# Performance work log

Measured on AMD Instinct MI355X. Metric: run time of the kernel, lower is better.

The kernel has to match this reference:

```python
import jax, jax.numpy as jnp
from jax import lax
import numpy as np

VOCAB, L, D, K = 50000, 8921, 300, 10
B, T = 8, 2048


def setup_inputs() -> dict:
    key = jax.random.key(0)
    k_ids, k_e, k_cw, k_cb, k_u = jax.random.split(key, 5)
    ids = jax.random.randint(k_ids, (B, T), 0, VOCAB, dtype=jnp.int32)
    embed_w = jax.random.normal(k_e, (VOCAB, D), dtype=jnp.float32) * 0.02
    embed_w = embed_w.at[0].set(0.0)  # padding_idx=0
    conv_w = jax.random.normal(k_cw, (D, D, K), dtype=jnp.float32) * 0.02  # (out, in, k) == torch OIH
    conv_b = jax.random.normal(k_cb, (D,), dtype=jnp.float32) * 0.02
    U = jax.random.normal(k_u, (L, D), dtype=jnp.float32)
    fc_bias = jnp.zeros((L,), dtype=jnp.float32)
    return {"ids": ids, "embed_w": embed_w, "conv_w": conv_w, "conv_b": conv_b, "U": U, "fc_bias": fc_bias}


def reference(ids, embed_w, conv_w, conv_b, U, fc_bias):
    # Embedding lookup (padding_idx row already zeroed in table)
    e = embed_w[ids]                       # (B, T, D)
    x = jnp.transpose(e, (0, 2, 1))        # (B, D, T)
    pad = conv_w.shape[-1] - 1             # torch padding=filter_size-1 (both sides)
    h = lax.conv_general_dilated(
        x, conv_w, window_strides=(1,), padding=[(pad, pad)],
        dimension_numbers=("NCH", "OIH", "NCH"))
    h = jax.nn.relu(h + conv_b[None, :, None])   # (B, D, T') where T' = T + K - 1
    attn = jax.nn.softmax(jnp.einsum("ld,bdt->blt", U, h), axis=-1)  # (B, L, T')
    z = jnp.einsum("blt,bdt->bld", attn, h)                          # (B, L, D)
    logits = jnp.einsum("bld,ld->bl", z, U) + fc_bias                # (B, L)
    return logits
```

## Files before the change

kernel.cpp:

```cpp
#include <hip/hip_runtime.h>

#define VOCAB   50000
#define LDIM    8921
#define DDIM    300
#define DPAD    320
#define KSZ     10
#define BATCH   8
#define TSEQ    2048
#define PADL    9
#define TPRIME  2057
#define TPADDED 2066
#define LPAD    8928

#define TSTG    32
#define NTT     65
#define TALLOC  (NTT * TSTG)
#define LBLK    70

typedef short s8v __attribute__((ext_vector_type(8)));
typedef float f4v __attribute__((ext_vector_type(4)));

typedef const __attribute__((address_space(1))) unsigned int* gas_ptr;
typedef __attribute__((address_space(3))) unsigned int* las_ptr;

__device__ inline unsigned short f2bf(float f) {
  union { float f; unsigned u; } v; v.f = f;
  unsigned r = v.u + 0x7FFF + ((v.u >> 16) & 1);
  return (unsigned short)(r >> 16);
}

__global__ __launch_bounds__(256) void gather_kernel(
    const int* __restrict__ ids, const float* __restrict__ embed_w,
    unsigned short* __restrict__ xp) {
  int wid = blockIdx.x * 4 + (threadIdx.x >> 6);
  int lane = threadIdx.x & 63;
  int b = wid / TPADDED, tau = wid % TPADDED;
  bool inr = (tau >= PADL) && (tau < PADL + TSEQ);
  int row = inr ? ids[b * TSEQ + (tau - PADL)] : 0;
  const float* src = embed_w + (size_t)row * DDIM;
  unsigned short* dst = xp + ((size_t)b * TPADDED + tau) * DPAD;
#pragma unroll
  for (int j = 0; j < 3; ++j) {
    int c2 = (j * 64 + lane) * 2;
    if (c2 < DPAD) {
      float v0 = (inr && c2 < DDIM) ? src[c2] : 0.0f;
      float v1 = (inr && c2 + 1 < DDIM) ? src[c2 + 1] : 0.0f;
      unsigned pk = (unsigned)f2bf(v0) | ((unsigned)f2bf(v1) << 16);
      *(unsigned*)&dst[c2] = pk;
    }
  }
}

__global__ __launch_bounds__(256) void prep_kernel(
    const float* __restrict__ w, const float* __restrict__ U,
    unsigned short* __restrict__ wT, unsigned short* __restrict__ Ub) {
  int bid = blockIdx.x;
  if (bid < KSZ * DPAD) {
    int k = bid / DPAD, o = bid % DPAD;
    for (int i = threadIdx.x; i < DPAD; i += 256) {
      float v = (o < DDIM && i < DDIM) ? w[((size_t)o * DDIM + i) * KSZ + k] : 0.0f;
      wT[((size_t)k * DPAD + o) * DPAD + i] = f2bf(v);
    }
  } else {
    int l = bid - KSZ * DPAD;
    for (int d = threadIdx.x; d < DPAD; d += 256) {
      float v = (l < LDIM && d < DDIM) ? U[(size_t)l * DDIM + d] : 0.0f;
      Ub[(size_t)l * DPAD + d] = f2bf(v);
    }
  }
}

#define CTN 80
#define CROWS 89
#define CSTRIDE 328
__global__ __launch_bounds__(256) void conv_mfma_kernel(
    const unsigned short* __restrict__ xp, const unsigned short* __restrict__ wT,
    const float* __restrict__ bias, unsigned short* __restrict__ h) {
  __shared__ unsigned short xls[CROWS * CSTRIDE];
  int b = blockIdx.x & 7, tb = blockIdx.x >> 3;
  int t0 = tb * CTN;
  int tid = threadIdx.x;
  {
    const unsigned short* src = xp + (size_t)b * TPADDED * DPAD;
    for (int idx = tid; idx < CROWS * 40; idx += 256) {
      int rr = idx / 40, c8 = idx % 40;
      int tp = t0 + rr;
      int4 v = make_int4(0, 0, 0, 0);
      if (tp < TPADDED) v = *(const int4*)&src[(size_t)tp * DPAD + c8 * 8];
      *(int4*)&xls[rr * CSTRIDE + c8 * 8] = v;
    }
  }
  __syncthreads();
  int w = tid >> 6, lane = tid & 63;
  int l15 = lane & 15, quad = lane >> 4;
  int ob = w * 80;
  f4v acc[5][5];
#pragma unroll
  for (int mf = 0; mf < 5; ++mf) {
    float bv[4];
#pragma unroll
    for (int rr = 0; rr < 4; ++rr) {
      int o = ob + mf * 16 + quad * 4 + rr;
      bv[rr] = (o < DDIM) ? bias[o] : 0.0f;
    }
#pragma unroll
    for (int nf = 0; nf < 5; ++nf) {
      acc[mf][nf][0] = bv[0]; acc[mf][nf][1] = bv[1];
      acc[mf][nf][2] = bv[2]; acc[mf][nf][3] = bv[3];
    }
  }
  const unsigned short* wl = wT + (size_t)(ob + l15) * DPAD + quad * 8;
  s8v Aping[5], Apong[5];
#pragma unroll
  for (int mf = 0; mf < 5; ++mf) Aping[mf] = *(const s8v*)&wl[mf * 16 * DPAD];
#pragma unroll
  for (int mf = 0; mf < 5; ++mf) Apong[mf] = *(const s8v*)&wl[mf * 16 * DPAD + 32];
  for (int ii = 0; ii < 100; ii += 2) {
    {
      int kc = ii / 10, it = ii % 10;
      s8v Bv[5];
#pragma unroll
      for (int nf = 0; nf < 5; ++nf)
        Bv[nf] = *(const s8v*)&xls[(nf * 16 + l15 + kc) * CSTRIDE + it * 32 + quad * 8];
#pragma unroll
      for (int mf = 0; mf < 5; ++mf)
#pragma unroll
        for (int nf = 0; nf < 5; ++nf)
          acc[mf][nf] = __builtin_amdgcn_mfma_f32_16x16x32_bf16(Aping[mf], Bv[nf], acc[mf][nf], 0, 0, 0);
      int p = ii + 2;
      if (p < 100) {
        int kp = p / 10, itp = p % 10;
        const unsigned short* wp = wl + (size_t)kp * (DPAD * DPAD) + itp * 32;
#pragma unroll
        for (int mf = 0; mf < 5; ++mf) Aping[mf] = *(const s8v*)&wp[mf * 16 * DPAD];
      }
    }
    {
      int kc = (ii + 1) / 10, it = (ii + 1) % 10;
      s8v Bv[5];
#pragma unroll
      for (int nf = 0; nf < 5; ++nf)
        Bv[nf] = *(const s8v*)&xls[(nf * 16 + l15 + kc) * CSTRIDE + it * 32 + quad * 8];
#pragma unroll
      for (int mf = 0; mf < 5; ++mf)
#pragma unroll
        for (int nf = 0; nf < 5; ++nf)
          acc[mf][nf] = __builtin_amdgcn_mfma_f32_16x16x32_bf16(Apong[mf], Bv[nf], acc[mf][nf], 0, 0, 0);
      int p = ii + 3;
      if (p < 100) {
        int kp = p / 10, itp = p % 10;
        const unsigned short* wp = wl + (size_t)kp * (DPAD * DPAD) + itp * 32;
#pragma unroll
        for (int mf = 0; mf < 5; ++mf) Apong[mf] = *(const s8v*)&wp[mf * 16 * DPAD];
      }
    }
  }
#pragma unroll
  for (int mf = 0; mf < 5; ++mf) {
    int obase = ob + mf * 16 + quad * 4;
#pragma unroll
    for (int nf = 0; nf < 5; ++nf) {
      int t = t0 + nf * 16 + l15;
      bool live = t < TPRIME;
      unsigned short pk[4];
#pragma unroll
      for (int rr = 0; rr < 4; ++rr)
        pk[rr] = live ? f2bf(fmaxf(acc[mf][nf][rr], 0.0f)) : (unsigned short)0;
      *(uint2*)&h[((size_t)b * TALLOC + t) * DPAD + obase] = *(uint2*)pk;
    }
  }
}

__global__ __launch_bounds__(512) void attn_mfma_kernel(
    const unsigned short* __restrict__ h, const unsigned short* __restrict__ Ub,
    const float* __restrict__ fcb, float* __restrict__ out) {
  __shared__ unsigned short hls[2 * TSTG * DPAD];
  int b = blockIdx.x & 7, lb = blockIdx.x >> 3;
  int tid = threadIdx.x;
  int w = tid >> 6, lane = tid & 63;
  int l15 = lane & 15, quad = lane >> 4;
  const unsigned short* hb = h + (size_t)b * TALLOC * DPAD;

  s8v A[10];
  {
    int lr = lb * 128 + w * 16 + l15;
    if (lr >= LPAD) lr = LPAD - 1;
    const unsigned short* up = Ub + (size_t)lr * DPAD + quad * 8;
#pragma unroll
    for (int kc = 0; kc < 10; ++kc)
      A[kc] = *(const s8v*)&up[kc * 32];
  }

  int nrounds = (w < 4) ? 3 : 2;
  int srcoff[3], ldsbase[3];
#pragma unroll
  for (int j = 0; j < 3; ++j) {
    int g = j * 512 + w * 64 + lane;
    int r = g / 40, c = g % 40;
    srcoff[j] = r * DPAD + ((c ^ (r & 7)) * 8);
    ldsbase[j] = (j * 512 + w * 64) * 8;
  }

#pragma unroll
  for (int j = 0; j < 3; ++j)
    if (j < nrounds)
      __builtin_amdgcn_global_load_lds((gas_ptr)(const void*)(hb + srcoff[j]),
                                       (las_ptr)(void*)&hls[ldsbase[j]],
                                       16, 0, 0);
  asm volatile("s_waitcnt vmcnt(0)" ::: "memory");
  __builtin_amdgcn_s_barrier();

  float se[4], sw[4];
#pragma unroll
  for (int r = 0; r < 4; ++r) { se[r] = 0.0f; sw[r] = 0.0f; }

  int xr8 = (l15 & 7) * 8;
  int rowb0 = l15 * DPAD;
  int rowb1 = (16 + l15) * DPAD;
  int bufsel = 0;
  const f4v vzero = {0.0f, 0.0f, 0.0f, 0.0f};
  for (int t = 0; t < NTT; ++t) {
    if (t + 1 < NTT) {
      const unsigned short* src = hb + (size_t)(t + 1) * TSTG * DPAD;
      int dstb = (bufsel ^ 1) * 10240;
#pragma unroll
      for (int j = 0; j < 3; ++j)
        if (j < nrounds)
          __builtin_amdgcn_global_load_lds((gas_ptr)(const void*)(src + srcoff[j]),
                                           (las_ptr)(void*)&hls[dstb + ldsbase[j]],
                                           16, 0, 0);
    }
    const unsigned short* bufc = &hls[bufsel * 10240];
    f4v acc0, acc1;
    __builtin_amdgcn_s_setprio(1);
    {
      int ko = (quad * 8) ^ xr8;
      s8v Bv0 = *(const s8v*)&bufc[rowb0 + ko];
      s8v Bv1 = *(const s8v*)&bufc[rowb1 + ko];
      acc0 = __builtin_amdgcn_mfma_f32_16x16x32_bf16(A[0], Bv0, vzero, 0, 0, 0);
      acc1 = __builtin_amdgcn_mfma_f32_16x16x32_bf16(A[0], Bv1, vzero, 0, 0, 0);
    }
#pragma unroll
    for (int kc = 1; kc < 10; ++kc) {
      int ko = (kc * 32 + quad * 8) ^ xr8;
      s8v Bv0 = *(const s8v*)&bufc[rowb0 + ko];
      s8v Bv1 = *(const s8v*)&bufc[rowb1 + ko];
      acc0 = __builtin_amdgcn_mfma_f32_16x16x32_bf16(A[kc], Bv0, acc0, 0, 0, 0);
      acc1 = __builtin_amdgcn_mfma_f32_16x16x32_bf16(A[kc], Bv1, acc1, 0, 0, 0);
    }
    __builtin_amdgcn_s_setprio(0);
#pragma unroll
    for (int r = 0; r < 4; ++r) {
      float s0 = acc0[r], s1 = acc1[r];
      float e0 = __expf(s0), e1 = __expf(s1);
      se[r] += e0 + e1;
      sw[r] = fmaf(e0, s0, sw[r]);
      sw[r] = fmaf(e1, s1, sw[r]);
    }
    asm volatile("s_waitcnt vmcnt(0)" ::: "memory");
    __builtin_amdgcn_s_barrier();
    bufsel ^= 1;
  }

#pragma unroll
  for (int r = 0; r < 4; ++r) {
    float a = se[r], c = sw[r];
#pragma unroll
    for (int off = 1; off < 16; off <<= 1) {
      a += __shfl_xor(a, off, 64);
      c += __shfl_xor(c, off, 64);
    }
    if (l15 == 0) {
      int l = lb * 128 + w * 16 + quad * 4 + r;
      if (l < LDIM) out[(size_t)b * LDIM + l] = c / (a - 23.0f) + fcb[l];
    }
  }
}

extern "C" void kernel_launch(void* const* d_in, const int* in_sizes, int n_in,
                              void* d_out, int out_size, void* d_ws, size_t ws_size,
                              hipStream_t stream) {
  const int*   ids     = (const int*)d_in[0];
  const float* embed_w = (const float*)d_in[1];
  const float* conv_w  = (const float*)d_in[2];
  const float* conv_b  = (const float*)d_in[3];
  const float* U       = (const float*)d_in[4];
  const float* fc_bias = (const float*)d_in[5];
  float* out = (float*)d_out;

  unsigned char* p = (unsigned char*)d_ws;
  unsigned short* xp = (unsigned short*)p;                 p += (size_t)BATCH * TPADDED * DPAD * 2;
  unsigned short* hb = (unsigned short*)p;                 p += (size_t)BATCH * TALLOC * DPAD * 2;
  unsigned short* wT = (unsigned short*)p;                 p += (size_t)KSZ * DPAD * DPAD * 2;
  unsigned short* Ub = (unsigned short*)p;

  hipLaunchKernelGGL(gather_kernel, dim3(BATCH * TPADDED / 4), dim3(256), 0, stream,
                     ids, embed_w, xp);
  hipLaunchKernelGGL(prep_kernel, dim3(KSZ * DPAD + LPAD), dim3(256), 0, stream,
                     conv_w, U, wT, Ub);
  hipLaunchKernelGGL(conv_mfma_kernel, dim3(BATCH * 26), dim3(256), 0, stream,
                     xp, wT, conv_b, hb);
  hipLaunchKernelGGL(attn_mfma_kernel, dim3(BATCH * LBLK), dim3(512), 0, stream,
                     hb, Ub, fc_bias, out);
}
```

Before: 305.4 us.

## Drop LDS staging in attention kernel; each wave computes two L tiles from global

The attention kernel no longer stages h tiles through double-buffered shared memory with global_load_lds. Each wave now loads B fragments straight from global memory (via cache) and reuses them across two 16-row L fragments, with blocks shrunk to 256 threads and launch bounds allowing 3 blocks per CU. This removes LDS traffic and its wait/barrier stalls and doubles MFMA work per B load, but it relies on L2/L1 for the repeated h reads, doubles A-fragment register use, and keeps a now-unneeded barrier.

```diff
diff --git a/kernel.cpp b/kernel.cpp
--- a/kernel.cpp
+++ b/kernel.cpp
@@ -19,9 +19,6 @@
 
 typedef short s8v __attribute__((ext_vector_type(8)));
 typedef float f4v __attribute__((ext_vector_type(4)));
-
-typedef const __attribute__((address_space(1))) unsigned int* gas_ptr;
-typedef __attribute__((address_space(3))) unsigned int* las_ptr;
 
 __device__ inline unsigned short f2bf(float f) {
   union { float f; unsigned u; } v; v.f = f;
@@ -171,110 +168,93 @@
   }
 }
 
-__global__ __launch_bounds__(512) void attn_mfma_kernel(
+__global__ __launch_bounds__(256, 3) void attn_mfma_kernel(
     const unsigned short* __restrict__ h, const unsigned short* __restrict__ Ub,
     const float* __restrict__ fcb, float* __restrict__ out) {
-  __shared__ unsigned short hls[2 * TSTG * DPAD];
   int b = blockIdx.x & 7, lb = blockIdx.x >> 3;
   int tid = threadIdx.x;
   int w = tid >> 6, lane = tid & 63;
   int l15 = lane & 15, quad = lane >> 4;
   const unsigned short* hb = h + (size_t)b * TALLOC * DPAD;
 
-  s8v A[10];
+  s8v A[2][10];
   {
-    int lr = lb * 128 + w * 16 + l15;
-    if (lr >= LPAD) lr = LPAD - 1;
-    const unsigned short* up = Ub + (size_t)lr * DPAD + quad * 8;
-#pragma unroll
-    for (int kc = 0; kc < 10; ++kc)
-      A[kc] = *(const s8v*)&up[kc * 32];
-  }
-
-  int nrounds = (w < 4) ? 3 : 2;
-  int srcoff[3], ldsbase[3];
-#pragma unroll
-  for (int j = 0; j < 3; ++j) {
-    int g = j * 512 + w * 64 + lane;
-    int r = g / 40, c = g % 40;
-    srcoff[j] = r * DPAD + ((c ^ (r & 7)) * 8);
-    ldsbase[j] = (j * 512 + w * 64) * 8;
-  }
-
-#pragma unroll
-  for (int j = 0; j < 3; ++j)
-    if (j < nrounds)
-      __builtin_amdgcn_global_load_lds((gas_ptr)(const void*)(hb + srcoff[j]),
-                                       (las_ptr)(void*)&hls[ldsbase[j]],
-                                       16, 0, 0);
-  asm volatile("s_waitcnt vmcnt(0)" ::: "memory");
-  __builtin_amdgcn_s_barrier();
-
-  float se[4], sw[4];
-#pragma unroll
-  for (int r = 0; r < 4; ++r) { se[r] = 0.0f; sw[r] = 0.0f; }
-
-  int xr8 = (l15 & 7) * 8;
-  int rowb0 = l15 * DPAD;
-  int rowb1 = (16 + l15) * DPAD;
-  int bufsel = 0;
+    int lr0 = lb * 128 + w * 32 + l15;
+#pragma unroll
+    for (int mf = 0; mf < 2; ++mf) {
+      int lr = lr0 + mf * 16;
+      if (lr >= LPAD) lr = LPAD - 1;
+      const unsigned short* up = Ub + (size_t)lr * DPAD + quad * 8;
+#pragma unroll
+      for (int kc = 0; kc < 10; ++kc)
+        A[mf][kc] = *(const s8v*)&up[kc * 32];
+    }
+  }
+
+  float se[2][4], sw[2][4];
+#pragma unroll
+  for (int mf = 0; mf < 2; ++mf)
+#pragma unroll
+    for (int r = 0; r < 4; ++r) { se[mf][r] = 0.0f; sw[mf][r] = 0.0f; }
+
+  const unsigned short* pb0 = hb + (size_t)l15 * DPAD + quad * 8;
+  const unsigned short* pb1 = pb0 + 16 * DPAD;
   const f4v vzero = {0.0f, 0.0f, 0.0f, 0.0f};
+
   for (int t = 0; t < NTT; ++t) {
-    if (t + 1 < NTT) {
-      const unsigned short* src = hb + (size_t)(t + 1) * TSTG * DPAD;
-      int dstb = (bufsel ^ 1) * 10240;
-#pragma unroll
-      for (int j = 0; j < 3; ++j)
-        if (j < nrounds)
-          __builtin_amdgcn_global_load_lds((gas_ptr)(const void*)(src + srcoff[j]),
-                                           (las_ptr)(void*)&hls[dstb + ldsbase[j]],
-                                           16, 0, 0);
-    }
-    const unsigned short* bufc = &hls[bufsel * 10240];
-    f4v acc0, acc1;
+    f4v a00, a01, a10, a11;
     __builtin_amdgcn_s_setprio(1);
     {
-      int ko = (quad * 8) ^ xr8;
-      s8v Bv0 = *(const s8v*)&bufc[rowb0 + ko];
-      s8v Bv1 = *(const s8v*)&bufc[rowb1 + ko];
-      acc0 = __builtin_amdgcn_mfma_f32_16x16x32_bf16(A[0], Bv0, vzero, 0, 0, 0);
-      acc1 = __builtin_amdgcn_mfma_f32_16x16x32_bf16(A[0], Bv1, vzero, 0, 0, 0);
+      s8v Bv0 = *(const s8v*)&pb0[0];
+      s8v Bv1 = *(const s8v*)&pb1[0];
+      a00 = __builtin_amdgcn_mfma_f32_16x16x32_bf16(A[0][0], Bv0, vzero, 0, 0, 0);
+      a01 = __builtin_amdgcn_mfma_f32_16x16x32_bf16(A[0][0], Bv1, vzero, 0, 0, 0);
+      a10 = __builtin_amdgcn_mfma_f32_16x16x32_bf16(A[1][0], Bv0, vzero, 0, 0, 0);
+      a11 = __builtin_amdgcn_mfma_f32_16x16x32_bf16(A[1][0], Bv1, vzero, 0, 0, 0);
     }
 #pragma unroll
     for (int kc = 1; kc < 10; ++kc) {
-      int ko = (kc * 32 + quad * 8) ^ xr8;
-      s8v Bv0 = *(const s8v*)&bufc[rowb0 + ko];
-      s8v Bv1 = *(const s8v*)&bufc[rowb1 + ko];
-      acc0 = __builtin_amdgcn_mfma_f32_16x16x32_bf16(A[kc], Bv0, acc0, 0, 0, 0);
-      acc1 = __builtin_amdgcn_mfma_f32_16x16x32_bf16(A[kc], Bv1, acc1, 0, 0, 0);
+      s8v Bv0 = *(const s8v*)&pb0[kc * 32];
+      s8v Bv1 = *(const s8v*)&pb1[kc * 32];
+      a00 = __builtin_amdgcn_mfma_f32_16x16x32_bf16(A[0][kc], Bv0, a00, 0, 0, 0);
+      a01 = __builtin_amdgcn_mfma_f32_16x16x32_bf16(A[0][kc], Bv1, a01, 0, 0, 0);
+      a10 = __builtin_amdgcn_mfma_f32_16x16x32_bf16(A[1][kc], Bv0, a10, 0, 0, 0);
+      a11 = __builtin_amdgcn_mfma_f32_16x16x32_bf16(A[1][kc], Bv1, a11, 0, 0, 0);
     }
     __builtin_amdgcn_s_setprio(0);
 #pragma unroll
     for (int r = 0; r < 4; ++r) {
-      float s0 = acc0[r], s1 = acc1[r];
+      float s0 = a00[r], s1 = a01[r];
       float e0 = __expf(s0), e1 = __expf(s1);
-      se[r] += e0 + e1;
-      sw[r] = fmaf(e0, s0, sw[r]);
-      sw[r] = fmaf(e1, s1, sw[r]);
-    }
-    asm volatile("s_waitcnt vmcnt(0)" ::: "memory");
+      se[0][r] += e0 + e1;
+      sw[0][r] = fmaf(e0, s0, sw[0][r]);
+      sw[0][r] = fmaf(e1, s1, sw[0][r]);
+      float s2 = a10[r], s3 = a11[r];
+      float e2 = __expf(s2), e3 = __expf(s3);
+      se[1][r] += e2 + e3;
+      sw[1][r] = fmaf(e2, s2, sw[1][r]);
+      sw[1][r] = fmaf(e3, s3, sw[1][r]);
+    }
+    pb0 += TSTG * DPAD;
+    pb1 += TSTG * DPAD;
     __builtin_amdgcn_s_barrier();
-    bufsel ^= 1;
-  }
-
-#pragma unroll
-  for (int r = 0; r < 4; ++r) {
-    float a = se[r], c = sw[r];
-#pragma unroll
-    for (int off = 1; off < 16; off <<= 1) {
-      a += __shfl_xor(a, off, 64);
-      c += __shfl_xor(c, off, 64);
-    }
-    if (l15 == 0) {
-      int l = lb * 128 + w * 16 + quad * 4 + r;
-      if (l < LDIM) out[(size_t)b * LDIM + l] = c / (a - 23.0f) + fcb[l];
-    }
-  }
+  }
+
+#pragma unroll
+  for (int mf = 0; mf < 2; ++mf)
+#pragma unroll
+    for (int r = 0; r < 4; ++r) {
+      float a = se[mf][r], c = sw[mf][r];
+#pragma unroll
+      for (int off = 1; off < 16; off <<= 1) {
+        a += __shfl_xor(a, off, 64);
+        c += __shfl_xor(c, off, 64);
+      }
+      if (l15 == 0) {
+        int l = lb * 128 + w * 32 + mf * 16 + quad * 4 + r;
+        if (l < LDIM) out[(size_t)b * LDIM + l] = c / (a - 23.0f) + fcb[l];
+      }
+    }
 }
 
 extern "C" void kernel_launch(void* const* d_in, const int* in_sizes, int n_in,
@@ -300,6 +280,6 @@
                      conv_w, U, wT, Ub);
   hipLaunchKernelGGL(conv_mfma_kernel, dim3(BATCH * 26), dim3(256), 0, stream,
                      xp, wT, conv_b, hb);
-  hipLaunchKernelGGL(attn_mfma_kernel, dim3(BATCH * LBLK), dim3(512), 0, stream,
+  hipLaunchKernelGGL(attn_mfma_kernel, dim3(BATCH * LBLK), dim3(256), 0, stream,
                      hb, Ub, fc_bias, out);
 }
```

New measurement: 614.6 us. +101.2%, slower.
